# Kernel optimization log

Measured on AMD Instinct MI355X. Metric: run time of the kernel, lower is better.

The kernel has to match this reference:

```python
import jax, jax.numpy as jnp
import numpy as np

V, H, O = 50257, 1024, 50257
B, T = 32, 512


def setup_inputs() -> dict:
    key = jax.random.key(0)
    ks = jax.random.split(key, 8)
    p = lambda k, shape: 0.02 * jax.random.normal(k, shape, dtype=jnp.float32)
    return {
        "state": jax.random.normal(ks[0], (B, H), dtype=jnp.float32),
        "tokens": jax.random.randint(ks[1], (B, T), 0, V, dtype=jnp.int64),
        "embedding": p(ks[2], (V, H)),
        "ih": p(ks[3], (H, H)),
        "hh": p(ks[4], (H, H)),
        "bias": p(ks[5], (H,)),
        "out_w": p(ks[6], (H, O)),
        "outBias": p(ks[7], (O,)),
    }


def reference(state, tokens, embedding, ih, hh, bias, out_w, outBias):
    # preCompute(): note torch broadcasts (H,H)/(H,) over the LAST axis,
    # i.e. column j is divided by ||hh[j,:]|| * H -- replicated faithfully.
    row_norms = jnp.linalg.norm(hh, axis=1)          # [H]
    scaledHH = hh / (row_norms * H)                  # [H,H]
    embedded = jnp.tanh(embedding) @ ih + bias       # [V,H]

    tokens_t = tokens.T                              # [T,B]

    def step(carry, tok):
        st, loss = carry                             # st: [B,H]
        logits = st @ out_w + outBias                # [B,O]
        logp = jax.nn.log_softmax(logits, axis=-1)
        nll = -jnp.take_along_axis(logp, tok[:, None], axis=1).mean()  # CE, mean over batch
        loss = loss + nll
        e = embedded[tok]                            # [B,H] gather
        # einsum('bi,bj->bi'): state scaled by sum over embedded features
        attn = jax.nn.softmax(st * e.sum(-1, keepdims=True), axis=-1)  # [B,H]
        st = jnp.tanh(st + attn @ scaledHH)
        return (st, loss), None

    (state, loss), _ = jax.lax.scan(step, (state, jnp.zeros((), state.dtype)), tokens_t)
    return state, loss
```

## Files before the change

### kernel.cpp

```cpp
#include <hip/hip_runtime.h>

#define VV 50257
#define HH 1024
#define OO 50257
#define BB 32
#define TT 512
#define NPAD2 50432
#define MROWS 16384
#define NBLK 32
#define KTILES 32

using bf16x8 = __attribute__((ext_vector_type(8))) short;
using f32x4  = __attribute__((ext_vector_type(4))) float;

__device__ __forceinline__ unsigned short f2bf(float x) {
    unsigned u = __float_as_uint(x);
    unsigned r = (u + 0x7FFFu + ((u >> 16) & 1u)) >> 16;
    return (unsigned short)r;
}
__device__ __forceinline__ float bf2f(unsigned short h) {
    return __uint_as_float(((unsigned)h) << 16);
}
__device__ __forceinline__ unsigned hz16(unsigned x) {
    return (x - 0x00010001u) & ~x & 0x80008000u;
}

__device__ __forceinline__ uint4 load_coh16(const void* p) {
    uint4 v;
    asm volatile("global_load_dwordx4 %0, %1, off sc0 sc1" : "=v"(v) : "v"(p));
    return v;
}
__device__ __forceinline__ void store_coh2(void* p, unsigned short s) {
    unsigned v = s;
    asm volatile("global_store_short %0, %1, off sc0 sc1" :: "v"(p), "v"(v) : "memory");
}
__device__ __forceinline__ void gload16(const void* g, void* l) {
    __builtin_amdgcn_global_load_lds((const __attribute__((address_space(1))) unsigned int*)g,
                                     (__attribute__((address_space(3))) unsigned int*)l, 16, 0, 0);
}

__global__ void prep_reduce(const float* __restrict__ ih, const float* __restrict__ hh,
                            const float* __restrict__ bias,
                            float* __restrict__ rs, float* __restrict__ rn, float* __restrict__ bsum) {
    int w = blockIdx.x * 4 + (threadIdx.x >> 6);
    int lane = threadIdx.x & 63;
    if (w < 1024) {
        const float* row = ih + (size_t)w * HH;
        float s = 0.f;
        for (int k = lane; k < HH; k += 64) s += row[k];
        for (int m = 1; m < 64; m <<= 1) s += __shfl_xor(s, m, 64);
        if (lane == 0) rs[w] = s;
    } else if (w < 2048) {
        int r = w - 1024;
        const float* row = hh + (size_t)r * HH;
        float s = 0.f;
        for (int k = lane; k < HH; k += 64) { float x = row[k]; s += x * x; }
        for (int m = 1; m < 64; m <<= 1) s += __shfl_xor(s, m, 64);
        if (lane == 0) rn[r] = sqrtf(s);
    } else if (w == 2048) {
        float s = 0.f;
        for (int k = lane; k < HH; k += 64) s += bias[k];
        for (int m = 1; m < 64; m <<= 1) s += __shfl_xor(s, m, 64);
        if (lane == 0) bsum[0] = s;
    }
}

__global__ void shconv(const float* __restrict__ hh, const float* __restrict__ rn,
                       unsigned short* __restrict__ SHb) {
    int gid = blockIdx.x * 256 + threadIdx.x;
    int slice = gid >> 12, kb = (gid >> 5) & 127, col = gid & 31;
    int j = slice * 32 + col;
    float inv = 1.0f / (rn[j] * 1024.0f);
    unsigned short v[8];
#pragma unroll
    for (int e = 0; e < 8; e++)
        v[e] = f2bf(hh[(size_t)(kb * 8 + e) * HH + j] * inv);
    uint4 pk;
    pk.x = (unsigned)v[0] | ((unsigned)v[1] << 16);
    pk.y = (unsigned)v[2] | ((unsigned)v[3] << 16);
    pk.z = (unsigned)v[4] | ((unsigned)v[5] << 16);
    pk.w = (unsigned)v[6] | ((unsigned)v[7] << 16);
    int gid_sw = (slice << 12) + (kb << 5) + (col ^ (kb & 3));
    *(uint4*)(SHb + (size_t)gid_sw * 8) = pk;
}

__global__ void esum_kernel(const float* __restrict__ emb, const float* __restrict__ rs,
                            const float* __restrict__ bsum, float* __restrict__ esum) {
    __shared__ float rs_l[HH];
    for (int i = threadIdx.x; i < HH; i += 256) rs_l[i] = rs[i];
    __syncthreads();
    int v = blockIdx.x * 4 + (threadIdx.x >> 6);
    if (v >= VV) return;
    int lane = threadIdx.x & 63;
    const float* row = emb + (size_t)v * HH;
    float s = 0.f;
    for (int k = lane; k < HH; k += 64) s += tanhf(row[k]) * rs_l[k];
    for (int m = 1; m < 64; m <<= 1) s += __shfl_xor(s, m, 64);
    if (lane == 0) esum[v] = s + bsum[0];
}

__global__ void esd_k(const int* __restrict__ tokens, const float* __restrict__ esum,
                      float* __restrict__ esd) {
    int idx = blockIdx.x * 256 + threadIdx.x;
    int t = idx >> 5, b = idx & 31;
    esd[idx] = esum[tokens[b * TT + t]];
}

__global__ void wconv(const float* __restrict__ W, unsigned short* __restrict__ Wb) {
    int n = blockIdx.x * 256 + threadIdx.x;
    int kb = blockIdx.y;
    unsigned short v[8];
#pragma unroll
    for (int e = 0; e < 8; e++) {
        float x = (n < OO) ? W[(size_t)(kb * 8 + e) * OO + n] : 0.0f;
        v[e] = f2bf(x);
    }
    uint4 pk;
    pk.x = (unsigned)v[0] | ((unsigned)v[1] << 16);
    pk.y = (unsigned)v[2] | ((unsigned)v[3] << 16);
    pk.z = (unsigned)v[4] | ((unsigned)v[5] << 16);
    pk.w = (unsigned)v[6] | ((unsigned)v[7] << 16);
    *(uint4*)(Wb + ((size_t)kb * NPAD2 + n) * 8) = pk;
}

__global__ void tokd_k(const int* __restrict__ tokens, int* __restrict__ tokd) {
    int r = blockIdx.x * 256 + threadIdx.x;
    int t = r >> 5, b = r & 31;
    tokd[r] = tokens[b * TT + t];
}

__global__ void __launch_bounds__(512) recurrence(
    const float* __restrict__ state_in, const unsigned short* __restrict__ SHb,
    const float* __restrict__ esd, unsigned short* __restrict__ S,
    unsigned short* __restrict__ abuf ,
    unsigned* __restrict__ flags ,
    float* __restrict__ out_state) {
    __shared__ unsigned short Wl[32768];
    __shared__ unsigned short Alds[32768];
    __shared__ f32x4 pacc[4][64];
    __shared__ float den_p[2][8][8];
    const int blk = blockIdx.x;
    const int tid = threadIdx.x;
    const int lane = tid & 63, w = tid >> 6;
    const int wr = (w >> 1) & 1, nt = w & 1, kh = w >> 2;
    const int q = lane >> 4, l16 = lane & 15;

    float st[4];
    const int b0 = wr * 16 + q * 4;
    const int jg = blk * 32 + nt * 16 + l16;
    if (kh == 0) {
#pragma unroll
        for (int r = 0; r < 4; r++) st[r] = state_in[(b0 + r) * HH + jg];
#pragma unroll
        for (int r = 0; r < 4; r++)
            store_coh2(abuf + (size_t)(b0 + r) * HH + jg, f2bf(__expf(st[r] * esd[b0 + r])));
        asm volatile("s_waitcnt vmcnt(0)" ::: "memory");
        if (lane == 0) {
            unsigned one = 1;
            asm volatile("global_store_dword %0, %1, off sc0 sc1"
                         :: "v"(flags + (blk * 4 + w) * 16), "v"(one) : "memory");
        }
    }
    {
        const uint4* src = (const uint4*)(SHb + (size_t)blk * 32768);
        uint4* dst = (uint4*)Wl;
#pragma unroll
        for (int i = 0; i < 8; i++) dst[tid + i * 512] = src[tid + i * 512];
    }

    for (int t = 0; t < TT; t++) {
        f32x4 es4;
        if (kh == 0) {
            int tn = (t < TT - 1) ? t + 1 : TT - 1;
            es4 = *(const f32x4*)&esd[tn * BB + b0];
#pragma unroll
            for (int r = 0; r < 4; r++)
                S[(size_t)(t * BB + b0 + r) * HH + jg] = f2bf(st[r]);
        }
        uint4 v[8];
        {
            const uint4* p0 = (const uint4*)abuf + (size_t)t * 4096 + tid;
            bool ok;
            int spins = 0;
            do {
#pragma unroll
                for (int i = 0; i < 8; i++) v[i] = load_coh16(p0 + i * 512);
                asm volatile("s_waitcnt vmcnt(0)" ::: "memory");
                __builtin_amdgcn_sched_barrier(0);
                unsigned bad = 0;
#pragma unroll
                for (int i = 0; i < 8; i++)
                    bad |= hz16(v[i].x) | hz16(v[i].y) | hz16(v[i].z) | hz16(v[i].w);
                ok = __all(bad == 0);
            } while (!ok && ++spins < 128);
            if (!ok) {
                const unsigned* f0 = flags + (2 * lane) * 16;
                const unsigned* f1 = flags + (2 * lane + 1) * 16;
                unsigned fa, fb;
                do {
                    asm volatile("global_load_dword %0, %2, off sc0 sc1\n\t"
                                 "global_load_dword %1, %3, off sc0 sc1\n\t"
                                 "s_waitcnt vmcnt(0)"
                                 : "=&v"(fa), "=&v"(fb) : "v"(f0), "v"(f1) : "memory");
                } while (!__all((int)(fa >= (unsigned)(t + 1) && fb >= (unsigned)(t + 1))));
#pragma unroll
                for (int i = 0; i < 8; i++) v[i] = load_coh16(p0 + i * 512);
                asm volatile("s_waitcnt vmcnt(0)" ::: "memory");
                __builtin_amdgcn_sched_barrier(0);
            }
        }
        float p[8];
#pragma unroll
        for (int i = 0; i < 8; i++) {
            int c = tid + i * 512;
            int byte = c * 16;
            int row = byte >> 11;
            *(uint4*)((char*)Alds + (byte ^ ((row & 7) << 4))) = v[i];
            float s = 0.f;
            const unsigned short* hp = (const unsigned short*)&v[i];
#pragma unroll
            for (int e = 0; e < 8; e++) s += bf2f(hp[e]);
            p[i] = s;
        }
#pragma unroll
        for (int i = 0; i < 8; i++) {
            float s = p[i];
            for (int m = 1; m < 64; m <<= 1) s += __shfl_xor(s, m, 64);
            p[i] = s;
        }
        if (lane == 0) {
#pragma unroll
            for (int i = 0; i < 8; i++) den_p[t & 1][w][i] = p[i];
        }
        __syncthreads();
        f32x4 acc = {0.f, 0.f, 0.f, 0.f};
#pragma unroll 4
        for (int kt = kh * 16; kt < kh * 16 + 16; kt++) {
            int arow = wr * 16 + l16;
            int abyte = (arow << 11) + kt * 64 + q * 16;
            abyte ^= (arow & 7) << 4;
            bf16x8 af = *(const bf16x8*)((const char*)Alds + abyte);
            int bbyte = ((kt * 4 + q) << 9) + (((nt * 16 + l16) ^ q) << 4);
            bf16x8 bfv = *(const bf16x8*)((const char*)Wl + bbyte);
            acc = __builtin_amdgcn_mfma_f32_16x16x32_bf16(af, bfv, acc, 0, 0, 0);
        }
        const int tile = wr * 2 + nt;
        if (kh == 1) pacc[tile][lane] = acc;
        __syncthreads();
        if (kh == 0) {
            f32x4 other = pacc[tile][lane];
            const bool last = (t == TT - 1);
#pragma unroll
            for (int r = 0; r < 4; r++) {
                float den = den_p[t & 1][2 * r][wr * 4 + q] + den_p[t & 1][2 * r + 1][wr * 4 + q];
                float u = (acc[r] + other[r]) / den;
                float stn = tanhf(st[r] + u);
                st[r] = stn;
                if (!last)
                    store_coh2(abuf + (size_t)(t + 1) * (BB * HH) +
                               (size_t)(b0 + r) * HH + jg, f2bf(__expf(stn * es4[r])));
            }
            if (!last) {
                asm volatile("s_waitcnt vmcnt(0)" ::: "memory");
                if (lane == 0) {
                    unsigned val = (unsigned)(t + 2);
                    asm volatile("global_store_dword %0, %1, off sc0 sc1"
                                 :: "v"(flags + (blk * 4 + w) * 16), "v"(val) : "memory");
                }
            }
        }
    }
    if (kh == 0) {
#pragma unroll
        for (int r = 0; r < 4; r++) out_state[(b0 + r) * HH + jg] = st[r];
    }
}

__global__ void __launch_bounds__(512) gemm_ce(
    const unsigned short* __restrict__ S, const unsigned short* __restrict__ Wb,
    const float* __restrict__ outBias, const int* __restrict__ tokd,
    float* __restrict__ Z, float* __restrict__ lt) {
    __shared__ unsigned short Ab[4][8192];
    __shared__ unsigned short Bb[4][8192];
    const int tid = threadIdx.x;
    const int lane = tid & 63, w = tid >> 6;
    const int wm = w >> 2, wn = w & 3;
    const int lin = blockIdx.x;
    const int id = (lin & 7) * 1576 + (lin >> 3);
    const int grp = id / (197 * 8);
    const int rem = id % (197 * 8);
    const int bx = rem >> 3;
    const int by = (grp << 3) + (rem & 7);
    const int bx256 = bx * 256, by256 = by * 256;

    const int arow = tid >> 2;
    const int rswA = (((tid & 3) ^ ((arow + (arow >> 2)) & 3)) << 3);
    const unsigned short* AsrcBase = S + (size_t)(by256 + arow) * 1024 + rswA;
    const unsigned short* BsrcBase = Wb + ((size_t)(tid >> 8) * NPAD2 + bx256 + (tid & 255)) * 8;

#define ISSUE_A(kt_) { unsigned short* d = Ab[(kt_) & 3];                         \
    const unsigned short* s0 = AsrcBase + (kt_) * 32;                             \
    gload16(s0, (char*)d + tid * 16);                                             \
    gload16(s0 + 128 * 1024, (char*)d + 8192 + tid * 16); }
#define ISSUE_B(kt_) { unsigned short* d = Bb[(kt_) & 3];                         \
    const unsigned short* s0 = BsrcBase + (size_t)(kt_) * 4 * NPAD2 * 8;          \
    gload16(s0, (char*)d + tid * 16);                                             \
    gload16(s0 + (size_t)2 * NPAD2 * 8, (char*)d + 8192 + tid * 16); }

    f32x4 acc[8][4];
#pragma unroll
    for (int mi = 0; mi < 8; mi++)
#pragma unroll
        for (int ni = 0; ni < 4; ni++) acc[mi][ni] = {0.f, 0.f, 0.f, 0.f};

    ISSUE_A(0); ISSUE_B(0); ISSUE_A(1); ISSUE_B(1); ISSUE_A(2); ISSUE_B(2);
    asm volatile("s_waitcnt vmcnt(8)" ::: "memory");
    __builtin_amdgcn_s_barrier();

    const int l15 = lane & 15;
    const int browA = wm * 128 + l15;
    const int slotA = (((lane >> 4) ^ ((browA + (browA >> 2)) & 3)) << 4);
    const int bcolB = ((lane >> 4) << 12) + ((wn * 64 + l15) << 4);

    for (int kt = 0; kt < KTILES; kt++) {
        const char* Abase = (const char*)Ab[kt & 3];
        const char* Bbase = (const char*)Bb[kt & 3];
        bf16x8 af[4], bf[4];
#pragma unroll
        for (int mi = 0; mi < 4; mi++)
            af[mi] = *(const bf16x8*)(Abase + ((browA + mi * 16) << 6) + slotA);
#pragma unroll
        for (int ni = 0; ni < 4; ni++)
            bf[ni] = *(const bf16x8*)(Bbase + bcolB + ni * 256);
        if (kt < KTILES - 3) ISSUE_A(kt + 3);
        __builtin_amdgcn_s_barrier();
        asm volatile("s_waitcnt lgkmcnt(0)" ::: "memory");
        __builtin_amdgcn_sched_barrier(0);
        __builtin_amdgcn_s_setprio(1);
#pragma unroll
        for (int mi = 0; mi < 4; mi++)
#pragma unroll
            for (int ni = 0; ni < 4; ni++)
                acc[mi][ni] = __builtin_amdgcn_mfma_f32_16x16x32_bf16(af[mi], bf[ni], acc[mi][ni], 0, 0, 0);
        __builtin_amdgcn_s_setprio(0);
        __builtin_amdgcn_s_barrier();
#pragma unroll
        for (int mi = 0; mi < 4; mi++)
            af[mi] = *(const bf16x8*)(Abase + ((browA + (mi + 4) * 16) << 6) + slotA);
        if (kt < KTILES - 3) ISSUE_B(kt + 3);
        __builtin_amdgcn_s_barrier();
        asm volatile("s_waitcnt lgkmcnt(0)" ::: "memory");
        __builtin_amdgcn_sched_barrier(0);
        __builtin_amdgcn_s_setprio(1);
#pragma unroll
        for (int mi = 0; mi < 4; mi++)
#pragma unroll
            for (int ni = 0; ni < 4; ni++)
                acc[mi + 4][ni] = __builtin_amdgcn_mfma_f32_16x16x32_bf16(af[mi], bf[ni], acc[mi + 4][ni], 0, 0, 0);
        __builtin_amdgcn_s_setprio(0);
        if (kt <= KTILES - 4) {
            asm volatile("s_waitcnt vmcnt(8)" ::: "memory");
        } else if (kt == KTILES - 3) {
            asm volatile("s_waitcnt vmcnt(4)" ::: "memory");
        } else if (kt == KTILES - 2) {
            asm volatile("s_waitcnt vmcnt(0)" ::: "memory");
        }
        __builtin_amdgcn_s_barrier();
    }
#undef ISSUE_A
#undef ISSUE_B

    const int colb = bx256 + wn * 64;
    const int rbase = by256 + wm * 128 + ((lane >> 4) << 2);
    float obv[4]; bool okv[4]; int jjv[4];
#pragma unroll
    for (int ni = 0; ni < 4; ni++) {
        jjv[ni] = colb + ni * 16 + l15;
        okv[ni] = jjv[ni] < OO;
        obv[ni] = okv[ni] ? outBias[jjv[ni]] : 0.f;
    }
    float rsum[8][4];
#pragma unroll
    for (int mi = 0; mi < 8; mi++)
#pragma unroll
        for (int r = 0; r < 4; r++) {
            int row = rbase + mi * 16 + r;
            int tk = tokd[row];
            float rssum = 0.f;
#pragma unroll
            for (int ni = 0; ni < 4; ni++) {
                float lg = acc[mi][ni][r] + obv[ni];
                rssum += okv[ni] ? __expf(lg) : 0.f;
                if (okv[ni] && jjv[ni] == tk) lt[row] = lg;
            }
            rsum[mi][r] = rssum;
        }
#pragma unroll
    for (int mi = 0; mi < 8; mi++)
#pragma unroll
        for (int r = 0; r < 4; r++) {
            float s = rsum[mi][r];
            s += __shfl_xor(s, 1, 64); s += __shfl_xor(s, 2, 64);
            s += __shfl_xor(s, 4, 64); s += __shfl_xor(s, 8, 64);
            rsum[mi][r] = s;
        }
    if (l15 == 0) {
#pragma unroll
        for (int mi = 0; mi < 8; mi++)
#pragma unroll
            for (int r = 0; r < 4; r++)
                atomicAdd(&Z[rbase + mi * 16 + r], rsum[mi][r]);
    }
}

__global__ void __launch_bounds__(1024) loss_reduce(const float* __restrict__ Z,
                                                    const float* __restrict__ lt,
                                                    float* __restrict__ out_loss) {
    __shared__ float red[16];
    float s = 0.f;
    for (int r = threadIdx.x; r < MROWS; r += 1024) s += logf(Z[r]) - lt[r];
    for (int m = 1; m < 64; m <<= 1) s += __shfl_xor(s, m, 64);
    if ((threadIdx.x & 63) == 0) red[threadIdx.x >> 6] = s;
    __syncthreads();
    if (threadIdx.x == 0) {
        float tot = 0.f;
        for (int q = 0; q < 16; q++) tot += red[q];
        out_loss[0] = tot / 32.0f;
    }
}

extern "C" void kernel_launch(void* const* d_in, const int* in_sizes, int n_in,
                              void* d_out, int out_size, void* d_ws, size_t ws_size,
                              hipStream_t stream) {
    const float* state  = (const float*)d_in[0];
    const int*   tokens = (const int*)d_in[1];
    const float* emb    = (const float*)d_in[2];
    const float* ih     = (const float*)d_in[3];
    const float* hh     = (const float*)d_in[4];
    const float* bias   = (const float*)d_in[5];
    const float* outw   = (const float*)d_in[6];
    const float* outb   = (const float*)d_in[7];

    char* ws = (char*)d_ws;
    size_t off = 0;
    auto alloc = [&](size_t bytes) { void* p = ws + off; off += (bytes + 255) & ~(size_t)255; return p; };
    unsigned short* Wb  = (unsigned short*)alloc((size_t)128 * NPAD2 * 8 * 2);
    unsigned short* S   = (unsigned short*)alloc((size_t)MROWS * HH * 2);
    unsigned short* abuf= (unsigned short*)alloc((size_t)TT * BB * HH * 2);
    unsigned short* SHb = (unsigned short*)alloc((size_t)131072 * 8 * 2);
    float* esum = (float*)alloc((size_t)VV * 4);
    float* esd  = (float*)alloc((size_t)MROWS * 4);
    float* rs   = (float*)alloc(4096);
    float* rn   = (float*)alloc(4096);
    float* bsum = (float*)alloc(256);
    float* Z    = (float*)alloc((size_t)MROWS * 4);
    float* lt   = (float*)alloc((size_t)MROWS * 4);
    int*   tokd = (int*)alloc((size_t)MROWS * 4);
    unsigned* flags = (unsigned*)alloc(128 * 16 * 4);
    float* out_state = (float*)d_out;
    float* out_loss  = out_state + 32768;

    hipMemsetAsync(Z, 0, (size_t)MROWS * 4, stream);
    hipMemsetAsync(abuf, 0, (size_t)TT * BB * HH * 2, stream);
    hipMemsetAsync(flags, 0, 128 * 16 * 4, stream);
    prep_reduce<<<513, 256, 0, stream>>>(ih, hh, bias, rs, rn, bsum);
    shconv<<<512, 256, 0, stream>>>(hh, rn, SHb);
    esum_kernel<<<12565, 256, 0, stream>>>(emb, rs, bsum, esum);
    esd_k<<<64, 256, 0, stream>>>(tokens, esum, esd);
    wconv<<<dim3(197, 128), 256, 0, stream>>>(outw, Wb);
    tokd_k<<<64, 256, 0, stream>>>(tokens, tokd);
    recurrence<<<NBLK, 512, 0, stream>>>(state, SHb, esd, S, abuf, flags, out_state);
    gemm_ce<<<64 * 197, 512, 0, stream>>>(S, Wb, outb, tokd, Z, lt);
    loss_reduce<<<1, 1024, 0, stream>>>(Z, lt, out_loss);
}
```

Before: 4.692 ms.

## Fuse recurrence and output GEMM into one persistent kernel with flag-gated tiles

Merges the sequential recurrence kernel and the vocab-projection GEMM+CE kernel into a single launch. The first 32 blocks run the recurrence and publish per-step progress flags. The remaining blocks persistently pull GEMM tiles from an atomic counter and spin on those flags until the needed rows of S have been written. This lets the large output GEMM overlap the latency-bound recurrence instead of waiting for it to finish. The cost is fewer GEMM blocks (persistent, 256 total), spin-waiting that competes for resources, and coherent S stores in the recurrence.

```diff
diff --git a/kernel.cpp b/kernel.cpp
--- a/kernel.cpp
+++ b/kernel.cpp
@@ -9,6 +9,7 @@
 #define MROWS 16384
 #define NBLK 32
 #define KTILES 32
+#define NTILES (64 * 197)
 
 using bf16x8 = __attribute__((ext_vector_type(8))) short;
 using f32x4  = __attribute__((ext_vector_type(4))) float;
@@ -129,287 +130,311 @@
     tokd[r] = tokens[b * TT + t];
 }
 
-__global__ void __launch_bounds__(512) recurrence(
+__global__ void __launch_bounds__(512) fused(
     const float* __restrict__ state_in, const unsigned short* __restrict__ SHb,
     const float* __restrict__ esd, unsigned short* __restrict__ S,
     unsigned short* __restrict__ abuf ,
     unsigned* __restrict__ flags ,
-    float* __restrict__ out_state) {
-    __shared__ unsigned short Wl[32768];
-    __shared__ unsigned short Alds[32768];
-    __shared__ f32x4 pacc[4][64];
-    __shared__ float den_p[2][8][8];
-    const int blk = blockIdx.x;
+    float* __restrict__ out_state,
+    const unsigned short* __restrict__ Wb, const float* __restrict__ outBias,
+    const int* __restrict__ tokd, float* __restrict__ Z, float* __restrict__ lt,
+    unsigned* __restrict__ wcnt ) {
+    __shared__ alignas(16) char smem[135680];
     const int tid = threadIdx.x;
     const int lane = tid & 63, w = tid >> 6;
-    const int wr = (w >> 1) & 1, nt = w & 1, kh = w >> 2;
-    const int q = lane >> 4, l16 = lane & 15;
-
-    float st[4];
-    const int b0 = wr * 16 + q * 4;
-    const int jg = blk * 32 + nt * 16 + l16;
-    if (kh == 0) {
-#pragma unroll
-        for (int r = 0; r < 4; r++) st[r] = state_in[(b0 + r) * HH + jg];
-#pragma unroll
-        for (int r = 0; r < 4; r++)
-            store_coh2(abuf + (size_t)(b0 + r) * HH + jg, f2bf(__expf(st[r] * esd[b0 + r])));
-        asm volatile("s_waitcnt vmcnt(0)" ::: "memory");
-        if (lane == 0) {
-            unsigned one = 1;
-            asm volatile("global_store_dword %0, %1, off sc0 sc1"
-                         :: "v"(flags + (blk * 4 + w) * 16), "v"(one) : "memory");
+
+    if (blockIdx.x < NBLK) {
+        unsigned short* Wl   = (unsigned short*)smem;
+        unsigned short* Alds = (unsigned short*)(smem + 65536);
+        f32x4 (*pacc)[64]    = (f32x4 (*)[64])(smem + 131072);
+        float (*den_p)[8][8] = (float (*)[8][8])(smem + 135168);
+        const int blk = blockIdx.x;
+        const int wr = (w >> 1) & 1, nt = w & 1, kh = w >> 2;
+        const int q = lane >> 4, l16 = lane & 15;
+
+        float st[4];
+        const int b0 = wr * 16 + q * 4;
+        const int jg = blk * 32 + nt * 16 + l16;
+        if (kh == 0) {
+#pragma unroll
+            for (int r = 0; r < 4; r++) st[r] = state_in[(b0 + r) * HH + jg];
+#pragma unroll
+            for (int r = 0; r < 4; r++)
+                store_coh2(abuf + (size_t)(b0 + r) * HH + jg, f2bf(__expf(st[r] * esd[b0 + r])));
+            asm volatile("s_waitcnt vmcnt(0)" ::: "memory");
+            if (lane == 0) {
+                unsigned one = 1;
+                asm volatile("global_store_dword %0, %1, off sc0 sc1"
+                             :: "v"(flags + (blk * 4 + w) * 16), "v"(one) : "memory");
+            }
         }
-    }
-    {
-        const uint4* src = (const uint4*)(SHb + (size_t)blk * 32768);
-        uint4* dst = (uint4*)Wl;
-#pragma unroll
-        for (int i = 0; i < 8; i++) dst[tid + i * 512] = src[tid + i * 512];
-    }
-
-    for (int t = 0; t < TT; t++) {
-        f32x4 es4;
+        {
+            const uint4* src = (const uint4*)(SHb + (size_t)blk * 32768);
+            uint4* dst = (uint4*)Wl;
+#pragma unroll
+            for (int i = 0; i < 8; i++) dst[tid + i * 512] = src[tid + i * 512];
+        }
+
+        for (int t = 0; t < TT; t++) {
+            f32x4 es4;
+            if (kh == 0) {
+                int tn = (t < TT - 1) ? t + 1 : TT - 1;
+                es4 = *(const f32x4*)&esd[tn * BB + b0];
+#pragma unroll
+                for (int r = 0; r < 4; r++)
+                    store_coh2(S + (size_t)(t * BB + b0 + r) * HH + jg, f2bf(st[r]));
+            }
+            uint4 v[8];
+            {
+                const uint4* p0 = (const uint4*)abuf + (size_t)t * 4096 + tid;
+                bool ok;
+                int spins = 0;
+                do {
+#pragma unroll
+                    for (int i = 0; i < 8; i++) v[i] = load_coh16(p0 + i * 512);
+                    asm volatile("s_waitcnt vmcnt(0)" ::: "memory");
+                    __builtin_amdgcn_sched_barrier(0);
+                    unsigned bad = 0;
+#pragma unroll
+                    for (int i = 0; i < 8; i++)
+                        bad |= hz16(v[i].x) | hz16(v[i].y) | hz16(v[i].z) | hz16(v[i].w);
+                    ok = __all(bad == 0);
+                } while (!ok && ++spins < 128);
+                if (!ok) {
+                    const unsigned* f0 = flags + (2 * lane) * 16;
+                    const unsigned* f1 = flags + (2 * lane + 1) * 16;
+                    unsigned fa, fb;
+                    do {
+                        asm volatile("global_load_dword %0, %2, off sc0 sc1\n\t"
+                                     "global_load_dword %1, %3, off sc0 sc1\n\t"
+                                     "s_waitcnt vmcnt(0)"
+                                     : "=&v"(fa), "=&v"(fb) : "v"(f0), "v"(f1) : "memory");
+                    } while (!__all((int)(fa >= (unsigned)(t + 1) && fb >= (unsigned)(t + 1))));
+#pragma unroll
+                    for (int i = 0; i < 8; i++) v[i] = load_coh16(p0 + i * 512);
+                    asm volatile("s_waitcnt vmcnt(0)" ::: "memory");
+                    __builtin_amdgcn_sched_barrier(0);
+                }
+            }
+            float p[8];
+#pragma unroll
+            for (int i = 0; i < 8; i++) {
+                int c = tid + i * 512;
+                int byte = c * 16;
+                int row = byte >> 11;
+                *(uint4*)((char*)Alds + (byte ^ ((row & 7) << 4))) = v[i];
+                float s = 0.f;
+                const unsigned short* hp = (const unsigned short*)&v[i];
+#pragma unroll
+                for (int e = 0; e < 8; e++) s += bf2f(hp[e]);
+                p[i] = s;
+            }
+#pragma unroll
+            for (int i = 0; i < 8; i++) {
+                float s = p[i];
+                for (int m = 1; m < 64; m <<= 1) s += __shfl_xor(s, m, 64);
+                p[i] = s;
+            }
+            if (lane == 0) {
+#pragma unroll
+                for (int i = 0; i < 8; i++) den_p[t & 1][w][i] = p[i];
+            }
+            __syncthreads();
+            f32x4 acc = {0.f, 0.f, 0.f, 0.f};
+#pragma unroll 4
+            for (int kt = kh * 16; kt < kh * 16 + 16; kt++) {
+                int arow = wr * 16 + l16;
+                int abyte = (arow << 11) + kt * 64 + q * 16;
+                abyte ^= (arow & 7) << 4;
+                bf16x8 af = *(const bf16x8*)((const char*)Alds + abyte);
+                int bbyte = ((kt * 4 + q) << 9) + (((nt * 16 + l16) ^ q) << 4);
+                bf16x8 bfv = *(const bf16x8*)((const char*)Wl + bbyte);
+                acc = __builtin_amdgcn_mfma_f32_16x16x32_bf16(af, bfv, acc, 0, 0, 0);
+            }
+            const int tile = wr * 2 + nt;
+            if (kh == 1) pacc[tile][lane] = acc;
+            __syncthreads();
+            if (kh == 0) {
+                f32x4 other = pacc[tile][lane];
+                const bool last = (t == TT - 1);
+#pragma unroll
+                for (int r = 0; r < 4; r++) {
+                    float den = den_p[t & 1][2 * r][wr * 4 + q] + den_p[t & 1][2 * r + 1][wr * 4 + q];
+                    float u = (acc[r] + other[r]) / den;
+                    float stn = tanhf(st[r] + u);
+                    st[r] = stn;
+                    if (!last)
+                        store_coh2(abuf + (size_t)(t + 1) * (BB * HH) +
+                                   (size_t)(b0 + r) * HH + jg, f2bf(__expf(stn * es4[r])));
+                }
+                if (!last) {
+                    asm volatile("s_waitcnt vmcnt(0)" ::: "memory");
+                    if (lane == 0) {
+                        unsigned val = (unsigned)(t + 2);
+                        asm volatile("global_store_dword %0, %1, off sc0 sc1"
+                                     :: "v"(flags + (blk * 4 + w) * 16), "v"(val) : "memory");
+                    }
+                }
+            }
+        }
         if (kh == 0) {
-            int tn = (t < TT - 1) ? t + 1 : TT - 1;
-            es4 = *(const f32x4*)&esd[tn * BB + b0];
-#pragma unroll
-            for (int r = 0; r < 4; r++)
-                S[(size_t)(t * BB + b0 + r) * HH + jg] = f2bf(st[r]);
+            asm volatile("s_waitcnt vmcnt(0)" ::: "memory");
+            if (lane == 0) {
+                unsigned val = 1000u;
+                asm volatile("global_store_dword %0, %1, off sc0 sc1"
+                             :: "v"(flags + (blk * 4 + w) * 16), "v"(val) : "memory");
+            }
+#pragma unroll
+            for (int r = 0; r < 4; r++) out_state[(b0 + r) * HH + jg] = st[r];
         }
-        uint4 v[8];
-        {
-            const uint4* p0 = (const uint4*)abuf + (size_t)t * 4096 + tid;
-            bool ok;
-            int spins = 0;
-            do {
-#pragma unroll
-                for (int i = 0; i < 8; i++) v[i] = load_coh16(p0 + i * 512);
-                asm volatile("s_waitcnt vmcnt(0)" ::: "memory");
-                __builtin_amdgcn_sched_barrier(0);
-                unsigned bad = 0;
-#pragma unroll
-                for (int i = 0; i < 8; i++)
-                    bad |= hz16(v[i].x) | hz16(v[i].y) | hz16(v[i].z) | hz16(v[i].w);
-                ok = __all(bad == 0);
-            } while (!ok && ++spins < 128);
-            if (!ok) {
+    } else {
+        char* AbB = smem;
+        char* BbB = smem + 65536;
+        unsigned* tileid = (unsigned*)(smem + 131072);
+        const int wm = w >> 2, wn = w & 3;
+        const int arow = tid >> 2;
+        const int rswA = (((tid & 3) ^ ((arow + (arow >> 2)) & 3)) << 3);
+        const int l15 = lane & 15;
+        const int browA = wm * 128 + l15;
+        const int slotA = (((lane >> 4) ^ ((browA + (browA >> 2)) & 3)) << 4);
+        const int bcolB = ((lane >> 4) << 12) + ((wn * 64 + l15) << 4);
+
+        for (;;) {
+            if (tid == 0) *tileid = atomicAdd(wcnt, 1u);
+            __syncthreads();
+            const unsigned id = *tileid;
+            if (id >= (unsigned)NTILES) break;
+            const int by = (int)(id / 197u), bx = (int)(id % 197u);
+            const int bx256 = bx * 256, by256 = by * 256;
+            if (w == 0) {
+                const unsigned need = (unsigned)(by * 8 + 9);
                 const unsigned* f0 = flags + (2 * lane) * 16;
                 const unsigned* f1 = flags + (2 * lane + 1) * 16;
-                unsigned fa, fb;
+                unsigned fa, fb; bool ok; int spins = 0;
                 do {
                     asm volatile("global_load_dword %0, %2, off sc0 sc1\n\t"
                                  "global_load_dword %1, %3, off sc0 sc1\n\t"
                                  "s_waitcnt vmcnt(0)"
                                  : "=&v"(fa), "=&v"(fb) : "v"(f0), "v"(f1) : "memory");
-                } while (!__all((int)(fa >= (unsigned)(t + 1) && fb >= (unsigned)(t + 1))));
-#pragma unroll
-                for (int i = 0; i < 8; i++) v[i] = load_coh16(p0 + i * 512);
-                asm volatile("s_waitcnt vmcnt(0)" ::: "memory");
+                    ok = __all((int)(fa >= need && fb >= need));
+                    if (!ok) __builtin_amdgcn_s_sleep(64);
+                } while (!ok && ++spins < (1 << 20));
+            }
+            __syncthreads();
+
+            const unsigned short* AsrcBase = S + (size_t)(by256 + arow) * 1024 + rswA;
+            const unsigned short* BsrcBase = Wb + ((size_t)(tid >> 8) * NPAD2 + bx256 + (tid & 255)) * 8;
+
+#define ISSUE_A(kt_) { char* d = AbB + ((kt_) & 3) * 16384;                       \
+    const unsigned short* s0 = AsrcBase + (kt_) * 32;                             \
+    gload16(s0, d + tid * 16);                                                    \
+    gload16(s0 + 128 * 1024, d + 8192 + tid * 16); }
+#define ISSUE_B(kt_) { char* d = BbB + ((kt_) & 3) * 16384;                       \
+    const unsigned short* s0 = BsrcBase + (size_t)(kt_) * 4 * NPAD2 * 8;          \
+    gload16(s0, d + tid * 16);                                                    \
+    gload16(s0 + (size_t)2 * NPAD2 * 8, d + 8192 + tid * 16); }
+
+            f32x4 acc[8][4];
+#pragma unroll
+            for (int mi = 0; mi < 8; mi++)
+#pragma unroll
+                for (int ni = 0; ni < 4; ni++) acc[mi][ni] = {0.f, 0.f, 0.f, 0.f};
+
+            ISSUE_A(0); ISSUE_B(0); ISSUE_A(1); ISSUE_B(1); ISSUE_A(2); ISSUE_B(2);
+            asm volatile("s_waitcnt vmcnt(8)" ::: "memory");
+            __builtin_amdgcn_s_barrier();
+
+            for (int kt = 0; kt < KTILES; kt++) {
+                const char* Abase = AbB + (kt & 3) * 16384;
+                const char* Bbase = BbB + (kt & 3) * 16384;
+                bf16x8 af[4], bf[4];
+#pragma unroll
+                for (int mi = 0; mi < 4; mi++)
+                    af[mi] = *(const bf16x8*)(Abase + ((browA + mi * 16) << 6) + slotA);
+#pragma unroll
+                for (int ni = 0; ni < 4; ni++)
+                    bf[ni] = *(const bf16x8*)(Bbase + bcolB + ni * 256);
+                if (kt < KTILES - 3) ISSUE_A(kt + 3);
+                __builtin_amdgcn_s_barrier();
+                asm volatile("s_waitcnt lgkmcnt(0)" ::: "memory");
                 __builtin_amdgcn_sched_barrier(0);
-            }
-        }
-        float p[8];
-#pragma unroll
-        for (int i = 0; i < 8; i++) {
-            int c = tid + i * 512;
-            int byte = c * 16;
-            int row = byte >> 11;
-            *(uint4*)((char*)Alds + (byte ^ ((row & 7) << 4))) = v[i];
-            float s = 0.f;
-            const unsigned short* hp = (const unsigned short*)&v[i];
-#pragma unroll
-            for (int e = 0; e < 8; e++) s += bf2f(hp[e]);
-            p[i] = s;
-        }
-#pragma unroll
-        for (int i = 0; i < 8; i++) {
-            float s = p[i];
-            for (int m = 1; m < 64; m <<= 1) s += __shfl_xor(s, m, 64);
-            p[i] = s;
-        }
-        if (lane == 0) {
-#pragma unroll
-            for (int i = 0; i < 8; i++) den_p[t & 1][w][i] = p[i];
-        }
-        __syncthreads();
-        f32x4 acc = {0.f, 0.f, 0.f, 0.f};
-#pragma unroll 4
-        for (int kt = kh * 16; kt < kh * 16 + 16; kt++) {
-            int arow = wr * 16 + l16;
-            int abyte = (arow << 11) + kt * 64 + q * 16;
-            abyte ^= (arow & 7) << 4;
-            bf16x8 af = *(const bf16x8*)((const char*)Alds + abyte);
-            int bbyte = ((kt * 4 + q) << 9) + (((nt * 16 + l16) ^ q) << 4);
-            bf16x8 bfv = *(const bf16x8*)((const char*)Wl + bbyte);
-            acc = __builtin_amdgcn_mfma_f32_16x16x32_bf16(af, bfv, acc, 0, 0, 0);
-        }
-        const int tile = wr * 2 + nt;
-        if (kh == 1) pacc[tile][lane] = acc;
-        __syncthreads();
-        if (kh == 0) {
-            f32x4 other = pacc[tile][lane];
-            const bool last = (t == TT - 1);
-#pragma unroll
-            for (int r = 0; r < 4; r++) {
-                float den = den_p[t & 1][2 * r][wr * 4 + q] + den_p[t & 1][2 * r + 1][wr * 4 + q];
-                float u = (acc[r] + other[r]) / den;
-                float stn = tanhf(st[r] + u);
-                st[r] = stn;
-                if (!last)
-                    store_coh2(abuf + (size_t)(t + 1) * (BB * HH) +
-                               (size_t)(b0 + r) * HH + jg, f2bf(__expf(stn * es4[r])));
-            }
-            if (!last) {
-                asm volatile("s_waitcnt vmcnt(0)" ::: "memory");
-                if (lane == 0) {
-                    unsigned val = (unsigned)(t + 2);
-                    asm volatile("global_store_dword %0, %1, off sc0 sc1"
-                                 :: "v"(flags + (blk * 4 + w) * 16), "v"(val) : "memory");
+                __builtin_amdgcn_s_setprio(1);
+#pragma unroll
+                for (int mi = 0; mi < 4; mi++)
+#pragma unroll
+                    for (int ni = 0; ni < 4; ni++)
+                        acc[mi][ni] = __builtin_amdgcn_mfma_f32_16x16x32_bf16(af[mi], bf[ni], acc[mi][ni], 0, 0, 0);
+                __builtin_amdgcn_s_setprio(0);
+                __builtin_amdgcn_s_barrier();
+#pragma unroll
+                for (int mi = 0; mi < 4; mi++)
+                    af[mi] = *(const bf16x8*)(Abase + ((browA + (mi + 4) * 16) << 6) + slotA);
+                if (kt < KTILES - 3) ISSUE_B(kt + 3);
+                __builtin_amdgcn_s_barrier();
+                asm volatile("s_waitcnt lgkmcnt(0)" ::: "memory");
+                __builtin_amdgcn_sched_barrier(0);
+                __builtin_amdgcn_s_setprio(1);
+#pragma unroll
+                for (int mi = 0; mi < 4; mi++)
+#pragma unroll
+                    for (int ni = 0; ni < 4; ni++)
+                        acc[mi + 4][ni] = __builtin_amdgcn_mfma_f32_16x16x32_bf16(af[mi], bf[ni], acc[mi + 4][ni], 0, 0, 0);
+                __builtin_amdgcn_s_setprio(0);
+                if (kt <= KTILES - 4) {
+                    asm volatile("s_waitcnt vmcnt(8)" ::: "memory");
+                } else if (kt == KTILES - 3) {
+                    asm volatile("s_waitcnt vmcnt(4)" ::: "memory");
+                } else if (kt == KTILES - 2) {
+                    asm volatile("s_waitcnt vmcnt(0)" ::: "memory");
                 }
-            }
-        }
-    }
-    if (kh == 0) {
-#pragma unroll
-        for (int r = 0; r < 4; r++) out_state[(b0 + r) * HH + jg] = st[r];
-    }
-}
-
-__global__ void __launch_bounds__(512) gemm_ce(
-    const unsigned short* __restrict__ S, const unsigned short* __restrict__ Wb,
-    const float* __restrict__ outBias, const int* __restrict__ tokd,
-    float* __restrict__ Z, float* __restrict__ lt) {
-    __shared__ unsigned short Ab[4][8192];
-    __shared__ unsigned short Bb[4][8192];
-    const int tid = threadIdx.x;
-    const int lane = tid & 63, w = tid >> 6;
-    const int wm = w >> 2, wn = w & 3;
-    const int lin = blockIdx.x;
-    const int id = (lin & 7) * 1576 + (lin >> 3);
-    const int grp = id / (197 * 8);
-    const int rem = id % (197 * 8);
-    const int bx = rem >> 3;
-    const int by = (grp << 3) + (rem & 7);
-    const int bx256 = bx * 256, by256 = by * 256;
-
-    const int arow = tid >> 2;
-    const int rswA = (((tid & 3) ^ ((arow + (arow >> 2)) & 3)) << 3);
-    const unsigned short* AsrcBase = S + (size_t)(by256 + arow) * 1024 + rswA;
-    const unsigned short* BsrcBase = Wb + ((size_t)(tid >> 8) * NPAD2 + bx256 + (tid & 255)) * 8;
-
-#define ISSUE_A(kt_) { unsigned short* d = Ab[(kt_) & 3];                         \
-    const unsigned short* s0 = AsrcBase + (kt_) * 32;                             \
-    gload16(s0, (char*)d + tid * 16);                                             \
-    gload16(s0 + 128 * 1024, (char*)d + 8192 + tid * 16); }
-#define ISSUE_B(kt_) { unsigned short* d = Bb[(kt_) & 3];                         \
-    const unsigned short* s0 = BsrcBase + (size_t)(kt_) * 4 * NPAD2 * 8;          \
-    gload16(s0, (char*)d + tid * 16);                                             \
-    gload16(s0 + (size_t)2 * NPAD2 * 8, (char*)d + 8192 + tid * 16); }
-
-    f32x4 acc[8][4];
-#pragma unroll
-    for (int mi = 0; mi < 8; mi++)
-#pragma unroll
-        for (int ni = 0; ni < 4; ni++) acc[mi][ni] = {0.f, 0.f, 0.f, 0.f};
-
-    ISSUE_A(0); ISSUE_B(0); ISSUE_A(1); ISSUE_B(1); ISSUE_A(2); ISSUE_B(2);
-    asm volatile("s_waitcnt vmcnt(8)" ::: "memory");
-    __builtin_amdgcn_s_barrier();
-
-    const int l15 = lane & 15;
-    const int browA = wm * 128 + l15;
-    const int slotA = (((lane >> 4) ^ ((browA + (browA >> 2)) & 3)) << 4);
-    const int bcolB = ((lane >> 4) << 12) + ((wn * 64 + l15) << 4);
-
-    for (int kt = 0; kt < KTILES; kt++) {
-        const char* Abase = (const char*)Ab[kt & 3];
-        const char* Bbase = (const char*)Bb[kt & 3];
-        bf16x8 af[4], bf[4];
-#pragma unroll
-        for (int mi = 0; mi < 4; mi++)
-            af[mi] = *(const bf16x8*)(Abase + ((browA + mi * 16) << 6) + slotA);
-#pragma unroll
-        for (int ni = 0; ni < 4; ni++)
-            bf[ni] = *(const bf16x8*)(Bbase + bcolB + ni * 256);
-        if (kt < KTILES - 3) ISSUE_A(kt + 3);
-        __builtin_amdgcn_s_barrier();
-        asm volatile("s_waitcnt lgkmcnt(0)" ::: "memory");
-        __builtin_amdgcn_sched_barrier(0);
-        __builtin_amdgcn_s_setprio(1);
-#pragma unroll
-        for (int mi = 0; mi < 4; mi++)
-#pragma unroll
-            for (int ni = 0; ni < 4; ni++)
-                acc[mi][ni] = __builtin_amdgcn_mfma_f32_16x16x32_bf16(af[mi], bf[ni], acc[mi][ni], 0, 0, 0);
-        __builtin_amdgcn_s_setprio(0);
-        __builtin_amdgcn_s_barrier();
-#pragma unroll
-        for (int mi = 0; mi < 4; mi++)
-            af[mi] = *(const bf16x8*)(Abase + ((browA + (mi + 4) * 16) << 6) + slotA);
-        if (kt < KTILES - 3) ISSUE_B(kt + 3);
-        __builtin_amdgcn_s_barrier();
-        asm volatile("s_waitcnt lgkmcnt(0)" ::: "memory");
-        __builtin_amdgcn_sched_barrier(0);
-        __builtin_amdgcn_s_setprio(1);
-#pragma unroll
-        for (int mi = 0; mi < 4; mi++)
-#pragma unroll
-            for (int ni = 0; ni < 4; ni++)
-                acc[mi + 4][ni] = __builtin_amdgcn_mfma_f32_16x16x32_bf16(af[mi], bf[ni], acc[mi + 4][ni], 0, 0, 0);
-        __builtin_amdgcn_s_setprio(0);
-        if (kt <= KTILES - 4) {
-            asm volatile("s_waitcnt vmcnt(8)" ::: "memory");
-        } else if (kt == KTILES - 3) {
-            asm volatile("s_waitcnt vmcnt(4)" ::: "memory");
-        } else if (kt == KTILES - 2) {
+                __builtin_amdgcn_s_barrier();
+            }
+#undef ISSUE_A
+#undef ISSUE_B
+
+            const int colb = bx256 + wn * 64;
+            const int rbase = by256 + wm * 128 + ((lane >> 4) << 2);
+            float obv[4]; bool okv[4]; int jjv[4];
+#pragma unroll
+            for (int ni = 0; ni < 4; ni++) {
+                jjv[ni] = colb + ni * 16 + l15;
+                okv[ni] = jjv[ni] < OO;
+                obv[ni] = okv[ni] ? outBias[jjv[ni]] : 0.f;
+            }
+            float rsum[8][4];
+#pragma unroll
+            for (int mi = 0; mi < 8; mi++)
+#pragma unroll
+                for (int r = 0; r < 4; r++) {
+                    int row = rbase + mi * 16 + r;
+                    int tk = tokd[row];
+                    float rssum = 0.f;
+#pragma unroll
+                    for (int ni = 0; ni < 4; ni++) {
+                        float lg = acc[mi][ni][r] + obv[ni];
+                        rssum += okv[ni] ? __expf(lg) : 0.f;
+                        if (okv[ni] && jjv[ni] == tk) lt[row] = lg;
+                    }
+                    rsum[mi][r] = rssum;
+                }
+#pragma unroll
+            for (int mi = 0; mi < 8; mi++)
+#pragma unroll
+                for (int r = 0; r < 4; r++) {
+                    float s = rsum[mi][r];
+                    s += __shfl_xor(s, 1, 64); s += __shfl_xor(s, 2, 64);
+                    s += __shfl_xor(s, 4, 64); s += __shfl_xor(s, 8, 64);
+                    rsum[mi][r] = s;
+                }
+            if (l15 == 0) {
+#pragma unroll
+                for (int mi = 0; mi < 8; mi++)
+#pragma unroll
+                    for (int r = 0; r < 4; r++)
+                        atomicAdd(&Z[rbase + mi * 16 + r], rsum[mi][r]);
+            }
             asm volatile("s_waitcnt vmcnt(0)" ::: "memory");
         }
-        __builtin_amdgcn_s_barrier();
-    }
-#undef ISSUE_A
-#undef ISSUE_B
-
-    const int colb = bx256 + wn * 64;
-    const int rbase = by256 + wm * 128 + ((lane >> 4) << 2);
-    float obv[4]; bool okv[4]; int jjv[4];
-#pragma unroll
-    for (int ni = 0; ni < 4; ni++) {
-        jjv[ni] = colb + ni * 16 + l15;
-        okv[ni] = jjv[ni] < OO;
-        obv[ni] = okv[ni] ? outBias[jjv[ni]] : 0.f;
-    }
-    float rsum[8][4];
-#pragma unroll
-    for (int mi = 0; mi < 8; mi++)
-#pragma unroll
-        for (int r = 0; r < 4; r++) {
-            int row = rbase + mi * 16 + r;
-            int tk = tokd[row];
-            float rssum = 0.f;
-#pragma unroll
-            for (int ni = 0; ni < 4; ni++) {
-                float lg = acc[mi][ni][r] + obv[ni];
-                rssum += okv[ni] ? __expf(lg) : 0.f;
-                if (okv[ni] && jjv[ni] == tk) lt[row] = lg;
-            }
-            rsum[mi][r] = rssum;
-        }
-#pragma unroll
-    for (int mi = 0; mi < 8; mi++)
-#pragma unroll
-        for (int r = 0; r < 4; r++) {
-            float s = rsum[mi][r];
-            s += __shfl_xor(s, 1, 64); s += __shfl_xor(s, 2, 64);
-            s += __shfl_xor(s, 4, 64); s += __shfl_xor(s, 8, 64);
-            rsum[mi][r] = s;
-        }
-    if (l15 == 0) {
-#pragma unroll
-        for (int mi = 0; mi < 8; mi++)
-#pragma unroll
-            for (int r = 0; r < 4; r++)
-                atomicAdd(&Z[rbase + mi * 16 + r], rsum[mi][r]);
     }
 }
 
@@ -457,19 +482,21 @@
     float* lt   = (float*)alloc((size_t)MROWS * 4);
     int*   tokd = (int*)alloc((size_t)MROWS * 4);
     unsigned* flags = (unsigned*)alloc(128 * 16 * 4);
+    unsigned* wcnt  = (unsigned*)alloc(256);
     float* out_state = (float*)d_out;
     float* out_loss  = out_state + 32768;
 
     hipMemsetAsync(Z, 0, (size_t)MROWS * 4, stream);
     hipMemsetAsync(abuf, 0, (size_t)TT * BB * HH * 2, stream);
     hipMemsetAsync(flags, 0, 128 * 16 * 4, stream);
+    hipMemsetAsync(wcnt, 0, 256, stream);
     prep_reduce<<<513, 256, 0, stream>>>(ih, hh, bias, rs, rn, bsum);
     shconv<<<512, 256, 0, stream>>>(hh, rn, SHb);
     esum_kernel<<<12565, 256, 0, stream>>>(emb, rs, bsum, esum);
     esd_k<<<64, 256, 0, stream>>>(tokens, esum, esd);
     wconv<<<dim3(197, 128), 256, 0, stream>>>(outw, Wb);
     tokd_k<<<64, 256, 0, stream>>>(tokens, tokd);
-    recurrence<<<NBLK, 512, 0, stream>>>(state, SHb, esd, S, abuf, flags, out_state);
-    gemm_ce<<<64 * 197, 512, 0, stream>>>(S, Wb, outb, tokd, Z, lt);
+    fused<<<256, 512, 0, stream>>>(state, SHb, esd, S, abuf, flags, out_state,
+                                   Wb, outb, tokd, Z, lt, wcnt);
     loss_reduce<<<1, 1024, 0, stream>>>(Z, lt, out_loss);
 }
```

After: 9.296 ms. 98.1% more time.
